# Kernel tuning notes

Measured on AMD Instinct MI355X. Metric: run time of the kernel, lower is better.

## Reference

```python
import jax, jax.numpy as jnp
import numpy as np

N, E, G = 50000, 640000, 1024
D, RD, H = 128, 200, 512
NUM_ATOM_FEATS, ATOM_VOCAB = 9, 64
NUM_BOND_FEATS, BOND_VOCAB = 3, 16


def setup_inputs() -> dict:
    key = jax.random.key(0)
    ks = jax.random.split(key, 24)
    inp = {
        "x_feat": jax.random.randint(ks[0], (N, NUM_ATOM_FEATS), 0, ATOM_VOCAB),
        "edge_index": jax.random.randint(ks[1], (2, E), 0, N),
        "edge_attr_feat": jax.random.randint(ks[2], (E, NUM_BOND_FEATS), 0, BOND_VOCAB),
        "batch": jnp.sort(jax.random.randint(ks[3], (N,), 0, G)),
        "rdkit_feats": jax.random.normal(ks[4], (G, RD), dtype=jnp.float32),
        # learned params
        "atom_emb": jax.random.normal(ks[5], (NUM_ATOM_FEATS, ATOM_VOCAB, D), dtype=jnp.float32) * 0.02,
        "bond_emb": jax.random.normal(ks[6], (NUM_BOND_FEATS, BOND_VOCAB, D), dtype=jnp.float32) * 0.02,
        "conv1_w1": jax.random.normal(ks[7], (D, D), dtype=jnp.float32) / np.sqrt(D),
        "conv1_b1": jnp.zeros((D,), jnp.float32),
        "conv1_w2": jax.random.normal(ks[8], (D, D), dtype=jnp.float32) / np.sqrt(D),
        "conv1_b2": jnp.zeros((D,), jnp.float32),
        "conv2_w1": jax.random.normal(ks[9], (D, D), dtype=jnp.float32) / np.sqrt(D),
        "conv2_b1": jnp.zeros((D,), jnp.float32),
        "conv2_w2": jax.random.normal(ks[10], (D, D), dtype=jnp.float32) / np.sqrt(D),
        "conv2_b2": jnp.zeros((D,), jnp.float32),
        "mlp_w1": jax.random.normal(ks[11], (D + RD, H), dtype=jnp.float32) / np.sqrt(D + RD),
        "mlp_b1": jnp.zeros((H,), jnp.float32),
        "mlp_w2": jax.random.normal(ks[12], (H, H // 2), dtype=jnp.float32) / np.sqrt(H),
        "mlp_b2": jnp.zeros((H // 2,), jnp.float32),
        "mlp_w3": jax.random.normal(ks[13], (H // 2, 1), dtype=jnp.float32) / np.sqrt(H // 2),
        "mlp_b3": jnp.zeros((1,), jnp.float32),
    }
    return inp


def _gine_conv(x, edge_index, edge_attr, w1, b1, w2, b2, eps=0.0):
    # PyG GINEConv: out = nn((1+eps)*x + sum_{j in N(i)} relu(x_j + e_ji))
    src, dst = edge_index[0], edge_index[1]
    msg = jax.nn.relu(x[src] + edge_attr)               # [E, D]
    agg = jax.ops.segment_sum(msg, dst, num_segments=x.shape[0])  # [N, D]
    h = (1.0 + eps) * x + agg
    h = jax.nn.relu(h @ w1 + b1)
    return h @ w2 + b2


def reference(x_feat, edge_index, edge_attr_feat, batch, rdkit_feats,
              atom_emb, bond_emb,
              conv1_w1, conv1_b1, conv1_w2, conv1_b2,
              conv2_w1, conv2_b1, conv2_w2, conv2_b2,
              mlp_w1, mlp_b1, mlp_w2, mlp_b2, mlp_w3, mlp_b3):
    # AtomEncoder / BondEncoder: sum of per-feature categorical embeddings
    x = atom_emb[jnp.arange(NUM_ATOM_FEATS)[None, :], x_feat].sum(axis=1)          # [N, D]
    edge_attr = bond_emb[jnp.arange(NUM_BOND_FEATS)[None, :], edge_attr_feat].sum(axis=1)  # [E, D]

    x = _gine_conv(x, edge_index, edge_attr, conv1_w1, conv1_b1, conv1_w2, conv1_b2)
    x = _gine_conv(x, edge_index, edge_attr, conv2_w1, conv2_b1, conv2_w2, conv2_b2)

    # global mean pool over graphs
    sums = jax.ops.segment_sum(x, batch, num_segments=G)                # [G, D]
    counts = jax.ops.segment_sum(jnp.ones((x.shape[0],), x.dtype), batch, num_segments=G)
    pooled = sums / jnp.maximum(counts, 1.0)[:, None]

    h = jnp.concatenate([pooled, rdkit_feats], axis=1)                  # [G, D+RD]
    h = jax.nn.relu(h @ mlp_w1 + mlp_b1)   # dropout is identity in eval mode
    h = jax.nn.relu(h @ mlp_w2 + mlp_b2)
    return h @ mlp_w3 + mlp_b3                                          # [G, 1]
```

## Files before the change

kernel.cpp:

```cpp
#include <hip/hip_runtime.h>

#define N_NODES 50000
#define N_EDGES 640000
#define N_GRAPH 1024
#define D 128
#define RD 200
#define CAP 64

typedef __attribute__((ext_vector_type(4))) float f32x4;
typedef __attribute__((ext_vector_type(8))) float f32x8;
typedef __attribute__((ext_vector_type(4))) _Float16 half4;
typedef __attribute__((ext_vector_type(8))) _Float16 half8;

__global__ void k_pre(const float* __restrict__ emb,
                      const int* __restrict__ xf, const int* __restrict__ batch,
                      const float* __restrict__ w0, const float* __restrict__ w1,
                      const float* __restrict__ w2, const float* __restrict__ w3,
                      const float* __restrict__ mw1, const float* __restrict__ mw2,
                      _Float16* __restrict__ cWf,
                      _Float16* __restrict__ W1f,
                      _Float16* __restrict__ W2f,
                      _Float16* __restrict__ x16, int* __restrict__ deg,
                      int* __restrict__ gstart) {
  if (blockIdx.x < 3125) {
    int t = blockIdx.x * 256 + threadIdx.x;
    int node = t >> 4, c = (t & 15) << 3;
    if ((t & 15) == 0) {
      int b = batch[node];
      int prev = (node == 0) ? -1 : batch[node - 1];
      for (int g = prev + 1; g <= b; ++g) gstart[g] = node;
      if (node == N_NODES - 1)
        for (int g = b + 1; g <= N_GRAPH; ++g) gstart[g] = N_NODES;
    }
    int v[9];
#pragma unroll
    for (int f = 0; f < 9; ++f) v[f] = xf[node * 9 + f];
    f32x8 a = (f32x8)(0.f);
#pragma unroll
    for (int f = 0; f < 9; ++f) {
      const float* er = &emb[(size_t)(f * 64 + v[f]) * D + c];
      float4 v0 = *(const float4*)er;
      float4 v1 = *(const float4*)(er + 4);
      a[0] += v0.x; a[1] += v0.y; a[2] += v0.z; a[3] += v0.w;
      a[4] += v1.x; a[5] += v1.y; a[6] += v1.z; a[7] += v1.w;
    }
    half8 o;
#pragma unroll
    for (int tt = 0; tt < 8; ++tt) o[tt] = (_Float16)a[tt];
    *(half8*)&x16[(size_t)node * D + c] = o;
  } else {
    int u = (blockIdx.x - 3125) * 256 + threadIdx.x;
    if (u < N_NODES) deg[u] = 0;
    if (u < 8192) {
      int mat = u >> 11, r = u & 2047;
      int frag = r >> 6, lane = r & 63;
      int n0 = frag >> 2, kk = frag & 3;
      int n = n0 * 16 + (lane & 15);
      int kb = (lane >> 4) * 8 + kk * 32;
      const float* W = (mat == 0) ? w0 : (mat == 1) ? w1 : (mat == 2) ? w2 : w3;
      half8 o;
#pragma unroll
      for (int j = 0; j < 8; ++j) o[j] = (_Float16)W[(kb + j) * D + n];
      *(half8*)&cWf[((size_t)mat * 2048 + r) * 8] = o;
    } else if (u < 8192 + 22528) {
      int t2 = u - 8192;
      int frag = t2 >> 6, lane = t2 & 63;
      int n0 = frag / 11, kk = frag % 11;
      int n = n0 * 16 + (lane & 15);
      int kb = (lane >> 4) * 8 + kk * 32;
      half8 o;
#pragma unroll
      for (int j = 0; j < 8; ++j) {
        int k = kb + j;
        o[j] = (k < 328) ? (_Float16)mw1[k * 512 + n] : (_Float16)0.f;
      }
      *(half8*)&W1f[(size_t)t2 * 8] = o;
    } else if (u < 8192 + 22528 + 16384) {
      int t2 = u - 8192 - 22528;
      int frag = t2 >> 6, lane = t2 & 63;
      int n0 = frag >> 4, kk = frag & 15;
      int n = n0 * 16 + (lane & 15);
      int kb = (lane >> 4) * 8 + kk * 32;
      half8 o;
#pragma unroll
      for (int j = 0; j < 8; ++j) o[j] = (_Float16)mw2[(kb + j) * 256 + n];
      *(half8*)&W2f[(size_t)t2 * 8] = o;
    }
  }
}

__global__ void k_fill(const int* __restrict__ ei, const int* __restrict__ bondf,
                       int* __restrict__ deg, int* __restrict__ csr1) {
  int e = blockIdx.x * 256 + threadIdx.x;
  if (e >= N_EDGES) return;
  int d = ei[N_EDGES + e];
  int rank = atomicAdd(&deg[d], 1);
  int s = ei[e];
  int f0 = bondf[e * 3], f1 = bondf[e * 3 + 1], f2 = bondf[e * 3 + 2];
  if (rank < CAP)
    csr1[(d << 6) | rank] = s | (f0 << 16) | (f1 << 20) | (f2 << 24);
}

__global__ __launch_bounds__(256) void k_agg(
    const _Float16* __restrict__ X, const int* __restrict__ deg,
    const int* __restrict__ csr1, const float* __restrict__ bemb,
    _Float16* __restrict__ out) {
  __shared__ half8 sB[48 * 16];
  for (int t = threadIdx.x; t < 768; t += blockDim.x) {
    float4 v0 = *(const float4*)&bemb[t * 8];
    float4 v1 = *(const float4*)&bemb[t * 8 + 4];
    half8 h;
    h[0] = (_Float16)v0.x; h[1] = (_Float16)v0.y; h[2] = (_Float16)v0.z; h[3] = (_Float16)v0.w;
    h[4] = (_Float16)v1.x; h[5] = (_Float16)v1.y; h[6] = (_Float16)v1.z; h[7] = (_Float16)v1.w;
    sB[t] = h;
  }
  __syncthreads();
  int lane = threadIdx.x & 63;
  int quad = lane >> 4, l15 = lane & 15, c8 = l15 * 8;
  int wid = blockIdx.x * 4 + (threadIdx.x >> 6);
  int nw = gridDim.x * 4;
  if (wid >= N_NODES) return;
  int pdeg = deg[wid];
  int pcreg = csr1[(wid << 6) + lane];
  for (int i = wid; i < N_NODES; i += nw) {
    int degn = pdeg;
    int creg = pcreg;
    int i2 = (i + nw < N_NODES) ? i + nw : i;
    pdeg = deg[i2];
    pcreg = csr1[(i2 << 6) + lane];
    int dq = degn > CAP ? CAP : degn;
    f32x8 ac0 = (f32x8)(0.f), ac1 = (f32x8)(0.f);
    for (int jb = 0; jb < dq; jb += 8) {
      unsigned e0v = (unsigned)__shfl(creg, jb + quad);
      unsigned e1v = (unsigned)__shfl(creg, jb + 4 + quad);
      if (jb + quad < dq) {
        half8 x0 = *(const half8*)&X[(size_t)(e0v & 0xFFFF) * D + c8];
        unsigned p0 = e0v >> 16;
        half8 m0h = (x0 + sB[(p0 & 15) * 16 + l15]) +
                    (sB[256 + ((p0 >> 4) & 15) * 16 + l15] + sB[512 + (p0 >> 8) * 16 + l15]);
        f32x8 g0 = __builtin_convertvector(m0h, f32x8);
#pragma unroll
        for (int tt = 0; tt < 8; ++tt) ac0[tt] += fmaxf(g0[tt], 0.f);
      }
      if (jb + 4 + quad < dq) {
        half8 x1 = *(const half8*)&X[(size_t)(e1v & 0xFFFF) * D + c8];
        unsigned p1 = e1v >> 16;
        half8 m1h = (x1 + sB[(p1 & 15) * 16 + l15]) +
                    (sB[256 + ((p1 >> 4) & 15) * 16 + l15] + sB[512 + (p1 >> 8) * 16 + l15]);
        f32x8 g1 = __builtin_convertvector(m1h, f32x8);
#pragma unroll
        for (int tt = 0; tt < 8; ++tt) ac1[tt] += fmaxf(g1[tt], 0.f);
      }
    }
    f32x8 acc = ac0 + ac1;
#pragma unroll
    for (int tt = 0; tt < 8; ++tt) {
      acc[tt] += __shfl_xor(acc[tt], 16);
      acc[tt] += __shfl_xor(acc[tt], 32);
    }
    if (quad == 0) {
      half8 sr = *(const half8*)&X[(size_t)i * D + c8];
      f32x8 o = __builtin_convertvector(sr, f32x8) + acc;
      half8 oh;
#pragma unroll
      for (int tt = 0; tt < 8; ++tt) oh[tt] = (_Float16)o[tt];
      *(half8*)&out[(size_t)i * D + c8] = oh;
    }
  }
}

__global__ __launch_bounds__(256) void k_conv(
    const _Float16* __restrict__ A,
    const _Float16* __restrict__ W1f, const float* __restrict__ b1,
    const _Float16* __restrict__ W2f, const float* __restrict__ b2,
    _Float16* __restrict__ O16) {
  __shared__ _Float16 sW[2048 * 8];
  __shared__ _Float16 sI[128 * 136];
  int tid = threadIdx.x, w = tid >> 6, lane = tid & 63;
  int m0 = blockIdx.x * 128;
  int col16 = lane & 15, q = lane >> 4;
  for (int t = tid; t < 2048; t += 256)
    *(float4*)&sW[t * 8] = *(const float4*)&W1f[(size_t)t * 8];
  half8 afr[2][4];
#pragma unroll
  for (int f = 0; f < 2; ++f) {
    int row = m0 + w * 32 + f * 16 + col16;
    if (row >= N_NODES) row = N_NODES - 1;
    const _Float16* Ar = A + (size_t)row * D + q * 8;
#pragma unroll
    for (int kk = 0; kk < 4; ++kk) afr[f][kk] = *(const half8*)(Ar + kk * 32);
  }
  __syncthreads();
#pragma unroll
  for (int n0 = 0; n0 < 8; ++n0) {
    f32x4 a0 = {0.f, 0.f, 0.f, 0.f}, a1 = {0.f, 0.f, 0.f, 0.f};
#pragma unroll
    for (int kk = 0; kk < 4; ++kk) {
      half8 b = *(const half8*)&sW[((n0 * 4 + kk) * 64 + lane) * 8];
      a0 = __builtin_amdgcn_mfma_f32_16x16x32_f16(afr[0][kk], b, a0, 0, 0, 0);
      a1 = __builtin_amdgcn_mfma_f32_16x16x32_f16(afr[1][kk], b, a1, 0, 0, 0);
    }
    float bb = b1[n0 * 16 + col16];
#pragma unroll
    for (int r = 0; r < 4; ++r) {
      sI[(w * 32 + q * 4 + r) * 136 + n0 * 16 + col16] = (_Float16)fmaxf(a0[r] + bb, 0.f);
      sI[(w * 32 + 16 + q * 4 + r) * 136 + n0 * 16 + col16] = (_Float16)fmaxf(a1[r] + bb, 0.f);
    }
  }
  __syncthreads();
  for (int t = tid; t < 2048; t += 256)
    *(float4*)&sW[t * 8] = *(const float4*)&W2f[(size_t)t * 8];
  half8 a2[2][4];
#pragma unroll
  for (int f = 0; f < 2; ++f) {
    const _Float16* tr = &sI[(w * 32 + f * 16 + col16) * 136 + q * 8];
#pragma unroll
    for (int kk = 0; kk < 4; ++kk) a2[f][kk] = *(const half8*)(tr + kk * 32);
  }
  __syncthreads();
#pragma unroll
  for (int n0 = 0; n0 < 8; ++n0) {
    f32x4 a0 = {0.f, 0.f, 0.f, 0.f}, a1 = {0.f, 0.f, 0.f, 0.f};
#pragma unroll
    for (int kk = 0; kk < 4; ++kk) {
      half8 b = *(const half8*)&sW[((n0 * 4 + kk) * 64 + lane) * 8];
      a0 = __builtin_amdgcn_mfma_f32_16x16x32_f16(a2[0][kk], b, a0, 0, 0, 0);
      a1 = __builtin_amdgcn_mfma_f32_16x16x32_f16(a2[1][kk], b, a1, 0, 0, 0);
    }
    int col = n0 * 16 + col16;
    float bb = b2[col];
#pragma unroll
    for (int r = 0; r < 4; ++r) {
      int r0 = m0 + w * 32 + q * 4 + r;
      int r1 = r0 + 16;
      if (r0 < N_NODES) O16[(size_t)r0 * D + col] = (_Float16)(a0[r] + bb);
      if (r1 < N_NODES) O16[(size_t)r1 * D + col] = (_Float16)(a1[r] + bb);
    }
  }
}

__global__ __launch_bounds__(512) void k_head(
    const _Float16* __restrict__ x, const int* __restrict__ gstart,
    const float* __restrict__ rdkit,
    const _Float16* __restrict__ W1f, const float* __restrict__ B1,
    const _Float16* __restrict__ W2f, const float* __restrict__ B2,
    const float* __restrict__ W3, const float* __restrict__ B3,
    float* __restrict__ out) {
  __shared__ _Float16 sH[16 * 360];
  __shared__ _Float16 sH1[16 * 520];
  int tid = threadIdx.x, w = tid >> 6, lane = tid & 63;
  int mt = blockIdx.x;
  int col16 = lane & 15, q = lane >> 4;

  {
    int half_ = lane >> 5;
    int c4 = (lane & 31) * 4;
#pragma unroll
    for (int gg = 0; gg < 2; ++gg) {
      int row = w * 2 + gg;
      int g = mt * 16 + row;
      int lo = gstart[g];
      int hi = gstart[g + 1];
      f32x4 a = {0.f, 0.f, 0.f, 0.f};
      for (int i = lo + half_; i < hi; i += 2) {
        half4 v = *(const half4*)&x[(size_t)i * D + c4];
        a += __builtin_convertvector(v, f32x4);
      }
#pragma unroll
      for (int t = 0; t < 4; ++t) a[t] += __shfl_xor(a[t], 32);
      float inv = 1.f / fmaxf((float)(hi - lo), 1.f);
      if (half_ == 0) {
        half4 o;
        o.x = (_Float16)(a[0] * inv); o.y = (_Float16)(a[1] * inv);
        o.z = (_Float16)(a[2] * inv); o.w = (_Float16)(a[3] * inv);
        *(half4*)&sH[row * 360 + c4] = o;
      }
      for (int r = lane; r < RD; r += 64)
        sH[row * 360 + D + r] = (_Float16)rdkit[(size_t)g * RD + r];
      if (lane < 24) sH[row * 360 + 328 + lane] = (_Float16)0.f;
      if (lane == 0) out[g] = B3[0];
    }
  }
  __syncthreads();

  {
    half8 afr[11];
    const _Float16* Ar = &sH[col16 * 360 + q * 8];
#pragma unroll
    for (int kk = 0; kk < 11; ++kk) afr[kk] = *(const half8*)(Ar + kk * 32);
#pragma unroll
    for (int ng = 0; ng < 4; ++ng) {
      int n0 = w * 4 + ng;
      f32x4 acc = {0.f, 0.f, 0.f, 0.f};
#pragma unroll
      for (int kk = 0; kk < 11; ++kk) {
        half8 b = *(const half8*)&W1f[(size_t)((n0 * 11 + kk) * 64 + lane) * 8];
        acc = __builtin_amdgcn_mfma_f32_16x16x32_f16(afr[kk], b, acc, 0, 0, 0);
      }
      int col = n0 * 16 + col16;
      float bb = B1[col];
#pragma unroll
      for (int r = 0; r < 4; ++r)
        sH1[(q * 4 + r) * 520 + col] = (_Float16)fmaxf(acc[r] + bb, 0.f);
    }
  }
  __syncthreads();

  {
    half8 a2[16];
    const _Float16* Ar = &sH1[col16 * 520 + q * 8];
#pragma unroll
    for (int kk = 0; kk < 16; ++kk) a2[kk] = *(const half8*)(Ar + kk * 32);
    float p[4] = {0.f, 0.f, 0.f, 0.f};
#pragma unroll
    for (int ng = 0; ng < 2; ++ng) {
      int n0 = w * 2 + ng;
      f32x4 acc = {0.f, 0.f, 0.f, 0.f};
#pragma unroll
      for (int kk = 0; kk < 16; ++kk) {
        half8 b = *(const half8*)&W2f[(size_t)((n0 * 16 + kk) * 64 + lane) * 8];
        acc = __builtin_amdgcn_mfma_f32_16x16x32_f16(a2[kk], b, acc, 0, 0, 0);
      }
      int col = n0 * 16 + col16;
      float bb = B2[col], w3 = W3[col];
#pragma unroll
      for (int r = 0; r < 4; ++r) p[r] += fmaxf(acc[r] + bb, 0.f) * w3;
    }
#pragma unroll
    for (int r = 0; r < 4; ++r) {
      p[r] += __shfl_xor(p[r], 1);
      p[r] += __shfl_xor(p[r], 2);
      p[r] += __shfl_xor(p[r], 4);
      p[r] += __shfl_xor(p[r], 8);
    }
    if (col16 == 0) {
#pragma unroll
      for (int r = 0; r < 4; ++r)
        atomicAdd(&out[mt * 16 + q * 4 + r], p[r]);
    }
  }
}

extern "C" void kernel_launch(void* const* d_in, const int* in_sizes, int n_in,
                              void* d_out, int out_size, void* d_ws, size_t ws_size,
                              hipStream_t stream) {
  const int* x_feat = (const int*)d_in[0];
  const int* ei = (const int*)d_in[1];
  const int* bondf = (const int*)d_in[2];
  const int* batch = (const int*)d_in[3];
  const float* rdkit = (const float*)d_in[4];
  const float* atom_emb = (const float*)d_in[5];
  const float* bond_emb = (const float*)d_in[6];
  const float* c1w1 = (const float*)d_in[7];
  const float* c1b1 = (const float*)d_in[8];
  const float* c1w2 = (const float*)d_in[9];
  const float* c1b2 = (const float*)d_in[10];
  const float* c2w1 = (const float*)d_in[11];
  const float* c2b1 = (const float*)d_in[12];
  const float* c2w2 = (const float*)d_in[13];
  const float* c2b2 = (const float*)d_in[14];
  const float* mw1 = (const float*)d_in[15];
  const float* mb1 = (const float*)d_in[16];
  const float* mw2 = (const float*)d_in[17];
  const float* mb2 = (const float*)d_in[18];
  const float* mw3 = (const float*)d_in[19];
  const float* mb3 = (const float*)d_in[20];
  float* out = (float*)d_out;

  char* ws = (char*)d_ws;
  size_t off = 0;
  auto alloc = [&](size_t bytes) {
    void* p = ws + off;
    off += (bytes + 255) & ~(size_t)255;
    return p;
  };
  _Float16* x16a = (_Float16*)alloc((size_t)N_NODES * D * 2);
  _Float16* x16b = (_Float16*)alloc((size_t)N_NODES * D * 2);
  _Float16* h16 = (_Float16*)alloc((size_t)N_NODES * D * 2);
  _Float16* x2_16 = (_Float16*)alloc((size_t)N_NODES * D * 2);
  int* deg = (int*)alloc((size_t)N_NODES * 4);
  int* csr1 = (int*)alloc((size_t)N_NODES * CAP * 4);
  int* gstart = (int*)alloc((size_t)(N_GRAPH + 1) * 4);
  _Float16* cWf = (_Float16*)alloc((size_t)4 * 2048 * 8 * 2);
  _Float16* W1f = (_Float16*)alloc((size_t)352 * 64 * 8 * 2);
  _Float16* W2f = (_Float16*)alloc((size_t)256 * 64 * 8 * 2);

  k_pre<<<3125 + 196, 256, 0, stream>>>(atom_emb, x_feat, batch,
                                        c1w1, c1w2, c2w1, c2w2, mw1, mw2,
                                        cWf, W1f, W2f, x16a, deg, gstart);
  k_fill<<<(N_EDGES + 255) / 256, 256, 0, stream>>>(ei, bondf, deg, csr1);

  int ctiles = (N_NODES + 127) / 128;
  k_agg<<<2048, 256, 0, stream>>>(x16a, deg, csr1, bond_emb, h16);
  k_conv<<<ctiles, 256, 0, stream>>>(h16, cWf + 0 * 16384, c1b1,
                                     cWf + 1 * 16384, c1b2, x16b);
  k_agg<<<2048, 256, 0, stream>>>(x16b, deg, csr1, bond_emb, h16);
  k_conv<<<ctiles, 256, 0, stream>>>(h16, cWf + 2 * 16384, c2b1,
                                     cWf + 3 * 16384, c2b2, x2_16);

  k_head<<<N_GRAPH / 16, 512, 0, stream>>>(x2_16, gstart, rdkit,
                                           W1f, mb1, W2f, mb2, mw3, mb3, out);

  (void)in_sizes; (void)n_in; (void)out_size; (void)ws_size;
}
```

Baseline: 275.6 us.

## Move degree atomics into k_pre and halve graphs per head block

The degree-counting atomics and edge packing move out of k_fill into extra blocks of k_pre, so they overlap with the atom embedding work. Each edge's destination, rank, source and bond features are staged in a new int2 buffer, and k_fill becomes a pure scatter into the CSR slots. The degree reset becomes a memset before k_pre. k_head now processes 8 graphs per block instead of 16, doubling the block count to spread pooling across more CUs, at the cost of wasting half of each MFMA tile on zero-padded rows.

Result: faster. 264.6 us (median of 2 runs) (-4.0%).

```diff
diff --git a/kernel.cpp b/kernel.cpp
--- a/kernel.cpp
+++ b/kernel.cpp
@@ -14,6 +14,7 @@
 
 __global__ void k_pre(const float* __restrict__ emb,
                       const int* __restrict__ xf, const int* __restrict__ batch,
+                      const int* __restrict__ ei, const int* __restrict__ bondf,
                       const float* __restrict__ w0, const float* __restrict__ w1,
                       const float* __restrict__ w2, const float* __restrict__ w3,
                       const float* __restrict__ mw1, const float* __restrict__ mw2,
@@ -21,7 +22,7 @@
                       _Float16* __restrict__ W1f,
                       _Float16* __restrict__ W2f,
                       _Float16* __restrict__ x16, int* __restrict__ deg,
-                      int* __restrict__ gstart) {
+                      int2* __restrict__ drep, int* __restrict__ gstart) {
   if (blockIdx.x < 3125) {
     int t = blockIdx.x * 256 + threadIdx.x;
     int node = t >> 4, c = (t & 15) << 3;
@@ -48,9 +49,15 @@
 #pragma unroll
     for (int tt = 0; tt < 8; ++tt) o[tt] = (_Float16)a[tt];
     *(half8*)&x16[(size_t)node * D + c] = o;
+  } else if (blockIdx.x < 5625) {
+    int e = (blockIdx.x - 3125) * 256 + threadIdx.x;
+    int d = ei[N_EDGES + e];
+    int rank = atomicAdd(&deg[d], 1);
+    int s = ei[e];
+    int f0 = bondf[e * 3], f1 = bondf[e * 3 + 1], f2 = bondf[e * 3 + 2];
+    drep[e] = make_int2(d | (rank << 16), s | (f0 << 16) | (f1 << 20) | (f2 << 24));
   } else {
-    int u = (blockIdx.x - 3125) * 256 + threadIdx.x;
-    if (u < N_NODES) deg[u] = 0;
+    int u = (blockIdx.x - 5625) * 256 + threadIdx.x;
     if (u < 8192) {
       int mat = u >> 11, r = u & 2047;
       int frag = r >> 6, lane = r & 63;
@@ -89,16 +96,13 @@
   }
 }
 
-__global__ void k_fill(const int* __restrict__ ei, const int* __restrict__ bondf,
-                       int* __restrict__ deg, int* __restrict__ csr1) {
+__global__ void k_fill(const int2* __restrict__ drep, int* __restrict__ csr1) {
   int e = blockIdx.x * 256 + threadIdx.x;
   if (e >= N_EDGES) return;
-  int d = ei[N_EDGES + e];
-  int rank = atomicAdd(&deg[d], 1);
-  int s = ei[e];
-  int f0 = bondf[e * 3], f1 = bondf[e * 3 + 1], f2 = bondf[e * 3 + 2];
-  if (rank < CAP)
-    csr1[(d << 6) | rank] = s | (f0 << 16) | (f1 << 20) | (f2 << 24);
+  int2 v = drep[e];
+  int d = v.x & 0xFFFF;
+  int rank = ((unsigned)v.x) >> 16;
+  if (rank < CAP) csr1[(d << 6) | rank] = v.y;
 }
 
 __global__ __launch_bounds__(256) void k_agg(
@@ -252,34 +256,33 @@
   int mt = blockIdx.x;
   int col16 = lane & 15, q = lane >> 4;
 
+  for (int t = tid; t < 2880; t += 512) sH[2880 + t] = (_Float16)0.f;
+
   {
+    int row = w;
+    int g = mt * 8 + w;
     int half_ = lane >> 5;
     int c4 = (lane & 31) * 4;
-#pragma unroll
-    for (int gg = 0; gg < 2; ++gg) {
-      int row = w * 2 + gg;
-      int g = mt * 16 + row;
-      int lo = gstart[g];
-      int hi = gstart[g + 1];
-      f32x4 a = {0.f, 0.f, 0.f, 0.f};
-      for (int i = lo + half_; i < hi; i += 2) {
-        half4 v = *(const half4*)&x[(size_t)i * D + c4];
-        a += __builtin_convertvector(v, f32x4);
-      }
-#pragma unroll
-      for (int t = 0; t < 4; ++t) a[t] += __shfl_xor(a[t], 32);
-      float inv = 1.f / fmaxf((float)(hi - lo), 1.f);
-      if (half_ == 0) {
-        half4 o;
-        o.x = (_Float16)(a[0] * inv); o.y = (_Float16)(a[1] * inv);
-        o.z = (_Float16)(a[2] * inv); o.w = (_Float16)(a[3] * inv);
-        *(half4*)&sH[row * 360 + c4] = o;
-      }
-      for (int r = lane; r < RD; r += 64)
-        sH[row * 360 + D + r] = (_Float16)rdkit[(size_t)g * RD + r];
-      if (lane < 24) sH[row * 360 + 328 + lane] = (_Float16)0.f;
-      if (lane == 0) out[g] = B3[0];
-    }
+    int lo = gstart[g];
+    int hi = gstart[g + 1];
+    f32x4 a = {0.f, 0.f, 0.f, 0.f};
+    for (int i = lo + half_; i < hi; i += 2) {
+      half4 v = *(const half4*)&x[(size_t)i * D + c4];
+      a += __builtin_convertvector(v, f32x4);
+    }
+#pragma unroll
+    for (int t = 0; t < 4; ++t) a[t] += __shfl_xor(a[t], 32);
+    float inv = 1.f / fmaxf((float)(hi - lo), 1.f);
+    if (half_ == 0) {
+      half4 o;
+      o.x = (_Float16)(a[0] * inv); o.y = (_Float16)(a[1] * inv);
+      o.z = (_Float16)(a[2] * inv); o.w = (_Float16)(a[3] * inv);
+      *(half4*)&sH[row * 360 + c4] = o;
+    }
+    for (int r = lane; r < RD; r += 64)
+      sH[row * 360 + D + r] = (_Float16)rdkit[(size_t)g * RD + r];
+    if (lane < 24) sH[row * 360 + 328 + lane] = (_Float16)0.f;
+    if (lane == 0) out[g] = B3[0];
   }
   __syncthreads();
 
@@ -333,10 +336,10 @@
       p[r] += __shfl_xor(p[r], 4);
       p[r] += __shfl_xor(p[r], 8);
     }
-    if (col16 == 0) {
+    if (col16 == 0 && q < 2) {
 #pragma unroll
       for (int r = 0; r < 4; ++r)
-        atomicAdd(&out[mt * 16 + q * 4 + r], p[r]);
+        atomicAdd(&out[mt * 8 + q * 4 + r], p[r]);
     }
   }
 }
@@ -380,15 +383,19 @@
   _Float16* x2_16 = (_Float16*)alloc((size_t)N_NODES * D * 2);
   int* deg = (int*)alloc((size_t)N_NODES * 4);
   int* csr1 = (int*)alloc((size_t)N_NODES * CAP * 4);
+  int2* drep = (int2*)alloc((size_t)N_EDGES * 8);
   int* gstart = (int*)alloc((size_t)(N_GRAPH + 1) * 4);
   _Float16* cWf = (_Float16*)alloc((size_t)4 * 2048 * 8 * 2);
   _Float16* W1f = (_Float16*)alloc((size_t)352 * 64 * 8 * 2);
   _Float16* W2f = (_Float16*)alloc((size_t)256 * 64 * 8 * 2);
 
-  k_pre<<<3125 + 196, 256, 0, stream>>>(atom_emb, x_feat, batch,
-                                        c1w1, c1w2, c2w1, c2w2, mw1, mw2,
-                                        cWf, W1f, W2f, x16a, deg, gstart);
-  k_fill<<<(N_EDGES + 255) / 256, 256, 0, stream>>>(ei, bondf, deg, csr1);
+  hipMemsetAsync(deg, 0, (size_t)N_NODES * 4, stream);
+  k_pre<<<3125 + 2500 + 196, 256, 0, stream>>>(atom_emb, x_feat, batch,
+                                               ei, bondf,
+                                               c1w1, c1w2, c2w1, c2w2, mw1, mw2,
+                                               cWf, W1f, W2f, x16a, deg, drep,
+                                               gstart);
+  k_fill<<<(N_EDGES + 255) / 256, 256, 0, stream>>>(drep, csr1);
 
   int ctiles = (N_NODES + 127) / 128;
   k_agg<<<2048, 256, 0, stream>>>(x16a, deg, csr1, bond_emb, h16);
@@ -398,8 +405,8 @@
   k_conv<<<ctiles, 256, 0, stream>>>(h16, cWf + 2 * 16384, c2b1,
                                      cWf + 3 * 16384, c2b2, x2_16);
 
-  k_head<<<N_GRAPH / 16, 512, 0, stream>>>(x2_16, gstart, rdkit,
-                                           W1f, mb1, W2f, mb2, mw3, mb3, out);
+  k_head<<<N_GRAPH / 8, 512, 0, stream>>>(x2_16, gstart, rdkit,
+                                          W1f, mb1, W2f, mb2, mw3, mb3, out);
 
   (void)in_sizes; (void)n_in; (void)out_size; (void)ws_size;
 }
```
